# Kernel tuning notes

Measured on AMD Instinct MI355X. Metric: run time of the kernel, lower is better.

Reference implementation:

```python
import jax, jax.numpy as jnp
import numpy as np

B, G, N, C = 4, 64, 256, 256
HEAD = 8
HD = C // HEAD  # 32


def setup_inputs() -> dict:
    key = jax.random.key(0)
    ks = jax.random.split(key, 11)
    s = 0.02
    return {
        "q": jax.random.normal(ks[0], (B, G, N, C), jnp.float32),
        "k": jax.random.normal(ks[1], (B, G, N, C), jnp.float32),
        "v": jax.random.normal(ks[2], (B, G, N, C), jnp.float32),
        "wq": jax.random.normal(ks[3], (C, C), jnp.float32) * s,
        "bq": jnp.zeros((C,), jnp.float32),
        "wk": jax.random.normal(ks[4], (C, C), jnp.float32) * s,
        "bk": jnp.zeros((C,), jnp.float32),
        "wv": jax.random.normal(ks[5], (C, C), jnp.float32) * s,
        "bv": jnp.zeros((C,), jnp.float32),
        "wo": jax.random.normal(ks[6], (C, C), jnp.float32) * s,
        "bo": jnp.zeros((C,), jnp.float32),
    }


def reference(q, k, v, wq, bq, wk, bk, wv, bv, wo, bo):
    # Linear projections (torch Linear == x @ W.T + b; here W stored as (in,out))
    Q = q @ wq + bq  # (B,G,N,C)
    K = k @ wk + bk
    V = v @ wv + bv
    # split heads: (B,G,N,C) -> (B,G,N,H,hd)
    Qh = Q.reshape(B, G, N, HEAD, HD)
    Kh = K.reshape(B, G, N, HEAD, HD)
    Vh = V.reshape(B, G, N, HEAD, HD)
    scale = jnp.sqrt(jnp.float32(HD)) + 1e-8
    # scores: per batch b, head h, group g: (N,N)
    score = jnp.einsum("bgnhd,bgmhd->bhgnm", Qh, Kh) / scale
    attn = jax.nn.softmax(score, axis=-1)
    ctx = jnp.einsum("bhgnm,bgmhd->bgnhd", attn, Vh)  # (B,G,N,H,hd)
    ctx = ctx.reshape(B, G, N, C)
    # output projection (dropout = identity in eval)
    return ctx @ wo + bo
```

## Files before the change

kernel.cpp:

```cpp
#include <hip/hip_runtime.h>
#include <hip/hip_bf16.h>
#include <cstdint>
#include <cstddef>


typedef __attribute__((ext_vector_type(4))) float f4;
typedef __attribute__((ext_vector_type(8))) short s8;
typedef __attribute__((ext_vector_type(4))) short s4;
typedef unsigned short u16;

#define AS1 __attribute__((address_space(1)))
#define AS3 __attribute__((address_space(3)))

static constexpr int CD = 256;

__device__ __forceinline__ u16 f2bf(float f) {
    __hip_bfloat16 h = __float2bfloat16(f);
    return *reinterpret_cast<u16*>(&h);
}

__device__ __forceinline__ void gload_lds16(const void* g, void* l) {
    __builtin_amdgcn_global_load_lds((const AS1 uint32_t*)g, (AS3 uint32_t*)l, 16, 0, 0);
}

__global__ __launch_bounds__(256) void prep_k(const float* __restrict__ wq,
                                              const float* __restrict__ wk,
                                              const float* __restrict__ wv,
                                              const float* __restrict__ wo,
                                              u16* __restrict__ WT, float qs)
{
    const int bx = blockIdx.x;
    const int wsel = bx >> 4, tl = bx & 15;
    const int k0 = (tl & 3) * 64, n0 = (tl >> 2) * 64;
    const float* W = wsel == 0 ? wq : wsel == 1 ? wk : wsel == 2 ? wv : wo;
    const float scale = wsel == 0 ? qs : 1.0f;
    u16* dst = WT + (size_t)wsel * 65536;
    __shared__ float T[64][65];
    const int t = threadIdx.x;
    const int rr = t >> 4, c0 = (t & 15) * 4;
    #pragma unroll
    for (int i = 0; i < 4; ++i) {
        int r = i * 16 + rr;
        f4 f = *(const f4*)(W + (size_t)(k0 + r) * CD + n0 + c0);
        #pragma unroll
        for (int j = 0; j < 4; ++j) T[c0 + j][r] = f[j] * scale;
    }
    __syncthreads();
    #pragma unroll
    for (int i = 0; i < 4; ++i) {
        int n = i * 16 + rr;
        s4 h;
        #pragma unroll
        for (int j = 0; j < 4; ++j) h[j] = (short)f2bf(T[n][c0 + j]);
        *(s4*)(dst + (size_t)(n0 + n) * CD + k0 + c0) = h;
    }
}

template<bool A_F32, bool OUT_F32>
__device__ __forceinline__ void gemm_body(const void* __restrict__ Ain,
                                          const u16* __restrict__ Wt,
                                          const float* __restrict__ bias,
                                          float escale, void* __restrict__ Out,
                                          int d)
{
    __shared__ u16 As[64 * 256];
    __shared__ u16 Bs[4][64 * 64];
    const int t = threadIdx.x, lane = t & 63, w = t >> 6;
    const int n0 = ((d >> 3) & 3) * 64;
    const int m0 = (((d >> 5) << 3) | (d & 7)) * 64;
    const int lr = lane & 15, lkg = lane >> 4;
    const int bc = lane >> 3, bcol = (lane & 7) * 8;

    f4 pf[16];
    if constexpr (A_F32) {
        const float* ap = (const float*)Ain + (size_t)(m0 + w * 16) * CD;
        #pragma unroll
        for (int j = 0; j < 16; ++j)
            pf[j] = *(const f4*)(ap + (size_t)j * CD + lane * 4);
    } else {
        const u16* A = (const u16*)Ain;
        #pragma unroll
        for (int j = 0; j < 8; ++j) {
            int ch = j * 256 + t;
            int row = ch >> 5, colb = (ch & 31) * 8;
            int col = colb ^ ((row & 7) << 3);
            gload_lds16(A + (size_t)(m0 + row) * CD + col, &As[ch * 8]);
        }
    }

    #pragma unroll
    for (int ck = 0; ck < 4; ++ck) {
        #pragma unroll
        for (int j = 0; j < 2; ++j) {
            int c = j * 4 + w;
            int row = c * 8 + bc;
            int col = bcol ^ ((row & 7) << 3);
            gload_lds16(Wt + (size_t)(n0 + row) * CD + ck * 64 + col,
                        &Bs[ck][c * 512 + lane * 8]);
        }
    }

    if constexpr (A_F32) {
        #pragma unroll
        for (int j = 0; j < 16; ++j) {
            int row = w * 16 + j;
            s4 h;
            #pragma unroll
            for (int i = 0; i < 4; ++i) h[i] = (short)f2bf(pf[j][i]);
            *(s4*)&As[row * 256 + ((lane * 4) ^ ((row & 7) << 3))] = h;
        }
    }

    __syncthreads();

    f4 acc[4] = {};
    #pragma unroll
    for (int ks = 0; ks < 8; ++ks) {
        int arow = w * 16 + lr;
        s8 a = *(const s8*)&As[arow * 256 +
                               ((ks * 32 + lkg * 8) ^ ((arow & 7) << 3))];
        const int ck = ks >> 1, kk = (ks & 1) * 32;
        #pragma unroll
        for (int n = 0; n < 4; ++n) {
            int R = n * 16 + lr;
            s8 b = *(const s8*)&Bs[ck][R * 64 + ((kk + lkg * 8) ^ ((R & 7) << 3))];
            acc[n] = __builtin_amdgcn_mfma_f32_16x16x32_bf16(a, b, acc[n], 0, 0, 0);
        }
    }

    const int orow = lkg * 4;
    #pragma unroll
    for (int n = 0; n < 4; ++n) {
        int col = n0 + n * 16 + lr;
        float bb = bias[col] * escale;
        #pragma unroll
        for (int r = 0; r < 4; ++r) {
            int row = m0 + w * 16 + orow + r;
            float vv = acc[n][r] + bb;
            if constexpr (OUT_F32)
                ((float*)Out)[(size_t)row * CD + col] = vv;
            else
                ((u16*)Out)[(size_t)row * CD + col] = f2bf(vv);
        }
    }
}

__global__ __launch_bounds__(256, 2) void gemmqkv_k(const float* q, const float* k,
        const float* v, const u16* WT, const float* bq, const float* bk,
        const float* bv, float qs, u16* Qb, u16* Kb, u16* Vb)
{
    const int op = blockIdx.x >> 12;
    const int d  = blockIdx.x & 4095;
    const float* A    = op == 0 ? q  : op == 1 ? k  : v;
    const u16*   Wt   = WT + (size_t)op * 65536;
    const float* bias = op == 0 ? bq : op == 1 ? bk : bv;
    u16*         Out  = op == 0 ? Qb : op == 1 ? Kb : Vb;
    gemm_body<true, false>(A, Wt, bias, op == 0 ? qs : 1.0f, Out, d);
}

__global__ __launch_bounds__(256, 2) void gemmo_k(const u16* Cx, const u16* WT,
                                                  const float* bo, float* out)
{
    gemm_body<false, true>(Cx, WT, bo, 1.0f, out, blockIdx.x);
}

__global__ __launch_bounds__(256, 3) void attn_k(const u16* Qb,
                                                 const u16* __restrict__ Kb,
                                                 const u16* __restrict__ Vb,
                                                 u16* Ctx)
{
    __shared__ u16 Ks[256 * 32];
    __shared__ u16 Vt[32][260];
    __shared__ u16 Ps[4][16][132];
    const int d = blockIdx.x;
    const int bg = d & 255, h = d >> 8;
    const size_t base = (size_t)bg * (256 * 256) + h * 32;
    const int t = threadIdx.x, lane = t & 63, w = t >> 6;
    const int lr = lane & 15, lk = (lane >> 4) * 8;
    const int orow = (lane >> 4) * 4;

    #pragma unroll
    for (int j = 0; j < 4; ++j) {
        int c = j * 4 + w;
        int row = c * 16 + (lane >> 2);
        int col = ((lane & 3) * 8) ^ (((row >> 1) & 3) << 3);
        gload_lds16(Kb + base + (size_t)row * CD + col, &Ks[c * 512 + lane * 8]);
    }
    {
        int n0 = (t >> 2) * 4, c0 = (t & 3) * 8;
        const u16* vp = Vb + base + (size_t)n0 * CD + c0;
        s8 r0 = *(const s8*)(vp);
        s8 r1 = *(const s8*)(vp + CD);
        s8 r2 = *(const s8*)(vp + 2 * CD);
        s8 r3 = *(const s8*)(vp + 3 * CD);
        #pragma unroll
        for (int i = 0; i < 8; ++i) {
            s4 cv = { r0[i], r1[i], r2[i], r3[i] };
            *(s4*)&Vt[c0 + i][n0] = cv;
        }
    }
    s8 aq[4];
    #pragma unroll
    for (int m = 0; m < 4; ++m)
        aq[m] = *(const s8*)(Qb + base + (size_t)(w * 64 + m * 16 + lr) * CD + lk);

    __syncthreads();

    const int myslot = lk ^ (((lr >> 1) & 3) << 3);
    const f4 zero = {0.f, 0.f, 0.f, 0.f};

    #pragma unroll
    for (int m = 0; m < 4; ++m) {
        f4 s[16];
        #pragma unroll
        for (int j = 0; j < 16; ++j) {
            s8 bk = *(const s8*)&Ks[(j * 16 + lr) * 32 + myslot];
            s[j] = __builtin_amdgcn_mfma_f32_16x16x32_bf16(aq[m], bk, zero, 0, 0, 0);
        }
        float mrow[4] = {-3.0e38f, -3.0e38f, -3.0e38f, -3.0e38f};
        #pragma unroll
        for (int j = 0; j < 16; ++j)
            #pragma unroll
            for (int r = 0; r < 4; ++r) mrow[r] = fmaxf(mrow[r], s[j][r]);
        #pragma unroll
        for (int dd = 1; dd < 16; dd <<= 1)
            #pragma unroll
            for (int r = 0; r < 4; ++r) mrow[r] = fmaxf(mrow[r], __shfl_xor(mrow[r], dd));
        float lsum[4] = {0.f, 0.f, 0.f, 0.f};
        #pragma unroll
        for (int j = 0; j < 16; ++j)
            #pragma unroll
            for (int r = 0; r < 4; ++r) {
                float p = exp2f(s[j][r] - mrow[r]);
                s[j][r] = p;
                lsum[r] += p;
            }
        #pragma unroll
        for (int dd = 1; dd < 16; dd <<= 1)
            #pragma unroll
            for (int r = 0; r < 4; ++r) lsum[r] += __shfl_xor(lsum[r], dd);

        f4 o0 = zero, o1 = zero;
        #pragma unroll
        for (int half = 0; half < 2; ++half) {
            #pragma unroll
            for (int j = 0; j < 8; ++j)
                #pragma unroll
                for (int r = 0; r < 4; ++r)
                    Ps[w][orow + r][j * 16 + lr] = f2bf(s[half * 8 + j][r]);
            #pragma unroll
            for (int kk = 0; kk < 4; ++kk) {
                s8 ap  = *(const s8*)&Ps[w][lr][kk * 32 + lk];
                s8 bv0 = *(const s8*)&Vt[lr][(half * 4 + kk) * 32 + lk];
                s8 bv1 = *(const s8*)&Vt[16 + lr][(half * 4 + kk) * 32 + lk];
                o0 = __builtin_amdgcn_mfma_f32_16x16x32_bf16(ap, bv0, o0, 0, 0, 0);
                o1 = __builtin_amdgcn_mfma_f32_16x16x32_bf16(ap, bv1, o1, 0, 0, 0);
            }
        }
        #pragma unroll
        for (int r = 0; r < 4; ++r) {
            float inv = __builtin_amdgcn_rcpf(lsum[r]);
            int row = w * 64 + m * 16 + orow + r;
            Ctx[base + (size_t)row * CD + lr]      = f2bf(o0[r] * inv);
            Ctx[base + (size_t)row * CD + 16 + lr] = f2bf(o1[r] * inv);
        }
    }
}

extern "C" void kernel_launch(void* const* d_in, const int* in_sizes, int n_in,
                              void* d_out, int out_size, void* d_ws, size_t ws_size,
                              hipStream_t stream) {
    const float* q  = (const float*)d_in[0];
    const float* k  = (const float*)d_in[1];
    const float* v  = (const float*)d_in[2];
    const float* wq = (const float*)d_in[3];
    const float* bq = (const float*)d_in[4];
    const float* wk = (const float*)d_in[5];
    const float* bk = (const float*)d_in[6];
    const float* wv = (const float*)d_in[7];
    const float* bv = (const float*)d_in[8];
    const float* wo = (const float*)d_in[9];
    const float* bo = (const float*)d_in[10];
    float* out = (float*)d_out;

    const size_t E = (size_t)65536 * 256;
    u16* Qb = (u16*)d_ws;
    u16* Kb = Qb + E;
    u16* Vb = Kb + E;
    u16* WT = Vb + E;
    u16* Cx = Qb;

    const float qs = (1.0f / (sqrtf(32.0f) + 1e-8f)) * 1.4426950408889634f;

    prep_k<<<64, 256, 0, stream>>>(wq, wk, wv, wo, WT, qs);
    gemmqkv_k<<<12288, 256, 0, stream>>>(q, k, v, WT, bq, bk, bv, qs, Qb, Kb, Vb);
    attn_k<<<2048, 256, 0, stream>>>(Qb, Kb, Vb, Cx);
    gemmo_k<<<4096, 256, 0, stream>>>(Cx, WT + 3 * 65536, bo, out);
}
```

Measured before the change: 206.2 us.

## Make projection GEMMs persistent with double-buffered A tiles and resident weights

Rewrites the QKV and output projection GEMMs as persistent kernels. Each block keeps its 64-column weight slice resident in LDS and loops over several 128-row panels of A. A is streamed in K-chunks of 32 through a double buffer, so global loads overlap the MFMA work. Bias add and output stores are vectorised, and the grids shrink to 768 and 512 blocks. This cuts repeated weight loads and launch overhead, at the cost of a barrier per K-chunk and less parallelism per kernel.

```diff
diff --git a/kernel.cpp b/kernel.cpp
--- a/kernel.cpp
+++ b/kernel.cpp
@@ -57,111 +57,184 @@
 }
 
 template<bool A_F32, bool OUT_F32>
-__device__ __forceinline__ void gemm_body(const void* __restrict__ Ain,
-                                          const u16* __restrict__ Wt,
-                                          const float* __restrict__ bias,
-                                          float escale, void* __restrict__ Out,
-                                          int d)
-{
-    __shared__ u16 As[64 * 256];
+__device__ __forceinline__ void gemm_persist(const void* __restrict__ Ain,
+                                             const u16* __restrict__ Wt,
+                                             const float* __restrict__ bias,
+                                             float escale, void* __restrict__ Out,
+                                             int n0, int mg, int npan, int mstride)
+{
     __shared__ u16 Bs[4][64 * 64];
+    __shared__ u16 As[2][128 * 32];
     const int t = threadIdx.x, lane = t & 63, w = t >> 6;
-    const int n0 = ((d >> 3) & 3) * 64;
-    const int m0 = (((d >> 5) << 3) | (d & 7)) * 64;
     const int lr = lane & 15, lkg = lane >> 4;
     const int bc = lane >> 3, bcol = (lane & 7) * 8;
-
-    f4 pf[16];
-    if constexpr (A_F32) {
-        const float* ap = (const float*)Ain + (size_t)(m0 + w * 16) * CD;
-        #pragma unroll
-        for (int j = 0; j < 16; ++j)
-            pf[j] = *(const f4*)(ap + (size_t)j * CD + lane * 4);
-    } else {
-        const u16* A = (const u16*)Ain;
-        #pragma unroll
-        for (int j = 0; j < 8; ++j) {
-            int ch = j * 256 + t;
-            int row = ch >> 5, colb = (ch & 31) * 8;
-            int col = colb ^ ((row & 7) << 3);
-            gload_lds16(A + (size_t)(m0 + row) * CD + col, &As[ch * 8]);
-        }
-    }
-
-    #pragma unroll
-    for (int ck = 0; ck < 4; ++ck) {
+    const int NG = npan * 8;
+
+    #pragma unroll
+    for (int ck = 0; ck < 4; ++ck)
         #pragma unroll
         for (int j = 0; j < 2; ++j) {
-            int c = j * 4 + w;
-            int row = c * 8 + bc;
-            int col = bcol ^ ((row & 7) << 3);
+            int c = j * 4 + w, row = c * 8 + bc, col = bcol ^ ((row & 7) << 3);
             gload_lds16(Wt + (size_t)(n0 + row) * CD + ck * 64 + col,
                         &Bs[ck][c * 512 + lane * 8]);
         }
-    }
-
-    if constexpr (A_F32) {
-        #pragma unroll
-        for (int j = 0; j < 16; ++j) {
-            int row = w * 16 + j;
-            s4 h;
-            #pragma unroll
-            for (int i = 0; i < 4; ++i) h[i] = (short)f2bf(pf[j][i]);
-            *(s4*)&As[row * 256 + ((lane * 4) ^ ((row & 7) << 3))] = h;
-        }
-    }
-
+
+    const float* Af = (const float*)Ain;
+    const u16*  Ab = (const u16*)Ain;
+
+    f4 rA0[4], rA1[4];
+
+    auto issue0 = [&](int g) {
+        int p = g >> 3, k0 = (g & 7) * 32;
+        size_t m0 = (size_t)(mg + p * mstride) * 128;
+        if constexpr (A_F32) {
+            #pragma unroll
+            for (int j = 0; j < 4; ++j) {
+                int ch = j * 256 + t, row = ch >> 3, c16 = ch & 7;
+                rA0[j] = *(const f4*)(Af + (m0 + row) * CD + k0 + c16 * 4);
+            }
+        } else {
+            #pragma unroll
+            for (int j = 0; j < 2; ++j) {
+                int rb = (w * 2 + j) * 16;
+                int row = rb + (lane >> 2), c0 = (lane & 3) * 8;
+                int scol = c0 ^ (((row >> 1) & 3) << 3);
+                gload_lds16(Ab + (m0 + row) * CD + k0 + scol,
+                            &As[0][rb * 32 + lane * 8]);
+            }
+        }
+    };
+    auto issue1 = [&](int g) {
+        int p = g >> 3, k0 = (g & 7) * 32;
+        size_t m0 = (size_t)(mg + p * mstride) * 128;
+        if constexpr (A_F32) {
+            #pragma unroll
+            for (int j = 0; j < 4; ++j) {
+                int ch = j * 256 + t, row = ch >> 3, c16 = ch & 7;
+                rA1[j] = *(const f4*)(Af + (m0 + row) * CD + k0 + c16 * 4);
+            }
+        } else {
+            #pragma unroll
+            for (int j = 0; j < 2; ++j) {
+                int rb = (w * 2 + j) * 16;
+                int row = rb + (lane >> 2), c0 = (lane & 3) * 8;
+                int scol = c0 ^ (((row >> 1) & 3) << 3);
+                gload_lds16(Ab + (m0 + row) * CD + k0 + scol,
+                            &As[1][rb * 32 + lane * 8]);
+            }
+        }
+    };
+    auto write0 = [&]() {
+        if constexpr (A_F32) {
+            #pragma unroll
+            for (int j = 0; j < 4; ++j) {
+                int ch = j * 256 + t, row = ch >> 3, c16 = ch & 7;
+                s4 h;
+                #pragma unroll
+                for (int i = 0; i < 4; ++i) h[i] = (short)f2bf(rA0[j][i]);
+                *(s4*)&As[0][row * 32 + ((c16 * 4) ^ (((row >> 1) & 3) << 3))] = h;
+            }
+        }
+    };
+    auto write1 = [&]() {
+        if constexpr (A_F32) {
+            #pragma unroll
+            for (int j = 0; j < 4; ++j) {
+                int ch = j * 256 + t, row = ch >> 3, c16 = ch & 7;
+                s4 h;
+                #pragma unroll
+                for (int i = 0; i < 4; ++i) h[i] = (short)f2bf(rA1[j][i]);
+                *(s4*)&As[1][row * 32 + ((c16 * 4) ^ (((row >> 1) & 3) << 3))] = h;
+            }
+        }
+    };
+
+    f4 acc[2][4] = {};
+
+    issue0(0);
+    write0();
     __syncthreads();
 
-    f4 acc[4] = {};
-    #pragma unroll
-    for (int ks = 0; ks < 8; ++ks) {
-        int arow = w * 16 + lr;
-        s8 a = *(const s8*)&As[arow * 256 +
-                               ((ks * 32 + lkg * 8) ^ ((arow & 7) << 3))];
-        const int ck = ks >> 1, kk = (ks & 1) * 32;
-        #pragma unroll
-        for (int n = 0; n < 4; ++n) {
-            int R = n * 16 + lr;
-            s8 b = *(const s8*)&Bs[ck][R * 64 + ((kk + lkg * 8) ^ ((R & 7) << 3))];
-            acc[n] = __builtin_amdgcn_mfma_f32_16x16x32_bf16(a, b, acc[n], 0, 0, 0);
-        }
-    }
-
-    const int orow = lkg * 4;
-    #pragma unroll
-    for (int n = 0; n < 4; ++n) {
-        int col = n0 + n * 16 + lr;
-        float bb = bias[col] * escale;
-        #pragma unroll
-        for (int r = 0; r < 4; ++r) {
-            int row = m0 + w * 16 + orow + r;
-            float vv = acc[n][r] + bb;
-            if constexpr (OUT_F32)
-                ((float*)Out)[(size_t)row * CD + col] = vv;
-            else
-                ((u16*)Out)[(size_t)row * CD + col] = f2bf(vv);
-        }
-    }
-}
-
-__global__ __launch_bounds__(256, 2) void gemmqkv_k(const float* q, const float* k,
+    for (int p = 0; p < npan; ++p) {
+        const size_t m0 = (size_t)(mg + p * mstride) * 128;
+        #pragma unroll
+        for (int c = 0; c < 8; ++c) {
+            const int g = p * 8 + c;
+            const bool haveNext = (g + 1 < NG);
+            if (haveNext) { if ((c & 1) == 0) issue1(g + 1); else issue0(g + 1); }
+            {
+                const int buf = c & 1;
+                const int ck = (g >> 1) & 3, kk = (g & 1) * 32;
+                s8 afr[2], bfr[4];
+                #pragma unroll
+                for (int m = 0; m < 2; ++m) {
+                    int row = w * 32 + m * 16 + lr;
+                    afr[m] = *(const s8*)&As[buf][row * 32 +
+                                 ((lkg * 8) ^ (((row >> 1) & 3) << 3))];
+                }
+                #pragma unroll
+                for (int n = 0; n < 4; ++n) {
+                    int R = n * 16 + lr;
+                    bfr[n] = *(const s8*)&Bs[ck][R * 64 +
+                                 ((kk + lkg * 8) ^ ((R & 7) << 3))];
+                }
+                #pragma unroll
+                for (int m = 0; m < 2; ++m)
+                    #pragma unroll
+                    for (int n = 0; n < 4; ++n)
+                        acc[m][n] = __builtin_amdgcn_mfma_f32_16x16x32_bf16(
+                            bfr[n], afr[m], acc[m][n], 0, 0, 0);
+            }
+            if (haveNext) { if ((c & 1) == 0) write1(); else write0(); }
+            if (c == 7) {
+                #pragma unroll
+                for (int m = 0; m < 2; ++m)
+                    #pragma unroll
+                    for (int n = 0; n < 4; ++n) {
+                        int col0 = n0 + n * 16 + lkg * 4;
+                        int row = (int)m0 + w * 32 + m * 16 + lr;
+                        f4 bb = *(const f4*)&bias[col0];
+                        f4 vv;
+                        #pragma unroll
+                        for (int r = 0; r < 4; ++r)
+                            vv[r] = acc[m][n][r] + bb[r] * escale;
+                        if constexpr (OUT_F32) {
+                            *(f4*)&((float*)Out)[(size_t)row * CD + col0] = vv;
+                        } else {
+                            s4 h;
+                            #pragma unroll
+                            for (int r = 0; r < 4; ++r) h[r] = (short)f2bf(vv[r]);
+                            *(s4*)&((u16*)Out)[(size_t)row * CD + col0] = h;
+                        }
+                        acc[m][n] = f4{0.f, 0.f, 0.f, 0.f};
+                    }
+            }
+            __syncthreads();
+        }
+    }
+}
+
+__global__ __launch_bounds__(256, 3) void gemmqkv_k(const float* q, const float* k,
         const float* v, const u16* WT, const float* bq, const float* bk,
         const float* bv, float qs, u16* Qb, u16* Kb, u16* Vb)
 {
-    const int op = blockIdx.x >> 12;
-    const int d  = blockIdx.x & 4095;
+    const int b = blockIdx.x;
+    const int op = b >> 8, r = b & 255;
+    const int n0 = ((r >> 6) & 3) * 64, mg = r & 63;
     const float* A    = op == 0 ? q  : op == 1 ? k  : v;
     const u16*   Wt   = WT + (size_t)op * 65536;
     const float* bias = op == 0 ? bq : op == 1 ? bk : bv;
     u16*         Out  = op == 0 ? Qb : op == 1 ? Kb : Vb;
-    gemm_body<true, false>(A, Wt, bias, op == 0 ? qs : 1.0f, Out, d);
+    gemm_persist<true, false>(A, Wt, bias, op == 0 ? qs : 1.0f, Out,
+                              n0, mg, 8, 64);
 }
 
 __global__ __launch_bounds__(256, 2) void gemmo_k(const u16* Cx, const u16* WT,
                                                   const float* bo, float* out)
 {
-    gemm_body<false, true>(Cx, WT, bo, 1.0f, out, blockIdx.x);
+    const int b = blockIdx.x;
+    const int n0 = (b >> 7) * 64, mg = b & 127;
+    gemm_persist<false, true>(Cx, WT, bo, 1.0f, out, n0, mg, 4, 128);
 }
 
 __global__ __launch_bounds__(256, 3) void attn_k(const u16* Qb,
@@ -293,7 +366,7 @@
     const float qs = (1.0f / (sqrtf(32.0f) + 1e-8f)) * 1.4426950408889634f;
 
     prep_k<<<64, 256, 0, stream>>>(wq, wk, wv, wo, WT, qs);
-    gemmqkv_k<<<12288, 256, 0, stream>>>(q, k, v, WT, bq, bk, bv, qs, Qb, Kb, Vb);
+    gemmqkv_k<<<768, 256, 0, stream>>>(q, k, v, WT, bq, bk, bv, qs, Qb, Kb, Vb);
     attn_k<<<2048, 256, 0, stream>>>(Qb, Kb, Vb, Cx);
-    gemmo_k<<<4096, 256, 0, stream>>>(Cx, WT + 3 * 65536, bo, out);
-}
+    gemmo_k<<<512, 256, 0, stream>>>(Cx, WT + 3 * 65536, bo, out);
+}
```

New measurement: 226.9 us. 1.1x slower.
